# Optimization experiments

Hardware: AMD Instinct MI355X
Metric: run time of the kernel (lower is better)

Reference implementation:

```python
import jax, jax.numpy as jnp
import numpy as np

M, N, K = 1024, 11008, 4096


def _unpack_i2u(Bp):
    """Unpack 2-bit unsigned weights per decode_i2u_to_i8s interleave.

    Bp: [N, K//4] int8 storage. Within each group of 4 bytes (16 elements),
    output element at position 4*i + j = (byte_j >> (2*i)) & 3.
    Returns [N, K] int8 with values in {0,1,2,3}.
    """
    Bu = jax.lax.bitcast_convert_type(Bp, jnp.uint8)  # [N, K//4]
    n, kc = Bu.shape
    Bg = Bu.reshape(n, kc // 4, 1, 4)                 # [N, G, 1, j]
    shifts = (jnp.arange(4, dtype=jnp.uint8) * jnp.uint8(2)).reshape(1, 1, 4, 1)
    vals = (Bg >> shifts) & jnp.uint8(3)              # [N, G, i, j]
    return vals.reshape(n, kc * 4).astype(jnp.int8)   # [N, K]


def setup_inputs() -> dict:
    key = jax.random.key(0)
    k1, k2 = jax.random.split(key)
    A = jax.random.randint(k1, (M, K), -128, 128, dtype=jnp.int8)
    B = jax.random.randint(k2, (N, K // 4), -128, 128, dtype=jnp.int8)
    return {"A": A, "B": B}


def reference(A, B):
    W = _unpack_i2u(B)  # [N, K] int8
    C = jax.lax.dot_general(
        A, W,
        dimension_numbers=(((1,), (1,)), ((), ())),
        preferred_element_type=jnp.int32,
    )  # [M, N] int32
    return C
```

## Files before the change

### kernel.cpp

```cpp
#include <hip/hip_runtime.h>
#include <stdint.h>


#define MM 1024
#define NN 11008
#define KK 4096
#define MTILES 8
#define NTILES 86
#define NBLOCKS (MTILES * NTILES)
#define STRIDE_A ((size_t)MTILES * 8192)
#define STRIDE_B ((size_t)NTILES * 2048)

using i32x4  = __attribute__((ext_vector_type(4))) int;
using i32x16 = __attribute__((ext_vector_type(16))) int;

__device__ __forceinline__ int pack4(i32x4 v) {
    return (int)(((uint32_t)v[0] & 0xFFu) | (((uint32_t)v[1] & 0xFFu) << 8)
               | (((uint32_t)v[2] & 0xFFu) << 16) | (((uint32_t)v[3] & 0xFFu) << 24));
}

__global__ __launch_bounds__(256) void prep_AB(const int* __restrict__ Asrc,
                                               const int* __restrict__ Bsrc,
                                               uint8_t* __restrict__ A2,
                                               uint8_t* __restrict__ B3) {
    if (blockIdx.x < 1024) {
        const int g = blockIdx.x * 256 + threadIdx.x;
        const int kstep = g >> 12;
        const int rem   = g & 4095;
        const int mtile = rem >> 9;
        const int c     = rem & 511;
        const int row32 = (c >> 7) & 3, kk2 = (c >> 6) & 1;
        const int lane  = c & 63;
        const int row   = mtile * 128 + row32 * 32 + (lane & 31);
        const int kbyte = kstep * 64 + kk2 * 32 + (lane >> 5) * 16;
        const i32x4* s4 = (const i32x4*)(Asrc + (size_t)row * KK + kbyte);
        i32x4 o;
#pragma unroll
        for (int q = 0; q < 4; ++q) o[q] = pack4(s4[q]);
        *(i32x4*)(A2 + (size_t)g * 16) = o;
    } else {
        const int t = (blockIdx.x - 1024) * 256 + threadIdx.x;
        const int n = t >> 6, kstep = t & 63;
        const int ntile = n >> 7, hf = (n >> 6) & 1, ni = (n >> 5) & 1, l31 = n & 31;
        const i32x4* s4 = (const i32x4*)(Bsrc + (size_t)n * (KK / 4) + kstep * 16);
        int w[4];
#pragma unroll
        for (int j = 0; j < 4; ++j) w[j] = pack4(s4[j]);
        uint8_t* base = B3 + ((size_t)kstep * NTILES + ntile) * 2048 + hf * 1024;
        *(int2*)(base + l31 * 16 + ni * 8)        = make_int2(w[0], w[2]);
        *(int2*)(base + (l31 + 32) * 16 + ni * 8) = make_int2(w[1], w[3]);
    }
}

#define GLOAD_LDS16(g, l) __builtin_amdgcn_global_load_lds(                    \
        (const __attribute__((address_space(1))) uint32_t*)(g),                \
        (__attribute__((address_space(3))) uint32_t*)(l), 16, 0, 0)

#define MFMA_I8 __builtin_amdgcn_mfma_i32_32x32x32_i8

#define PSTAGE(T) do {                                                         \
    const uint8_t* at_ = gA + (size_t)(T) * STRIDE_A;                          \
    const uint8_t* bt_ = gB + (size_t)(T) * STRIDE_B;                          \
    uint8_t* l_ = &As[(T) % 5][0];                                             \
    GLOAD_LDS16(at_,        l_);                                               \
    GLOAD_LDS16(at_ + 1024, l_ + 1024);                                        \
    GLOAD_LDS16(at_ + 2048, l_ + 2048);                                        \
    GLOAD_LDS16(at_ + 3072, l_ + 3072);                                        \
    GLOAD_LDS16(at_ + 4096, l_ + 4096);                                        \
    GLOAD_LDS16(at_ + 5120, l_ + 5120);                                        \
    GLOAD_LDS16(at_ + 6144, l_ + 6144);                                        \
    GLOAD_LDS16(at_ + 7168, l_ + 7168);                                        \
    GLOAD_LDS16(bt_,        l_ + 8192);                                        \
    GLOAD_LDS16(bt_ + 1024, l_ + 9216);                                        \
} while (0)

#define PWAIT(N) asm volatile("s_waitcnt vmcnt(" #N ")" ::: "memory")

#define READF(BUF, T) do {                                                     \
    const uint8_t* ab_ = &As[(T) % 5][0];                                      \
    BUF##_a00 = *(const i32x4*)(ab_ + (wr * 2 + 0) * 2048 + lane * 16);        \
    BUF##_a01 = *(const i32x4*)(ab_ + (wr * 2 + 0) * 2048 + 1024 + lane * 16); \
    BUF##_a10 = *(const i32x4*)(ab_ + (wr * 2 + 1) * 2048 + lane * 16);        \
    BUF##_a11 = *(const i32x4*)(ab_ + (wr * 2 + 1) * 2048 + 1024 + lane * 16); \
    BUF##_bv  = *(const i32x4*)(ab_ + 8192 + wc * 1024 + lane * 16);           \
} while (0)

#define COMPR(BUF) do {                                                        \
    _Pragma("unroll")                                                          \
    for (int kk2_ = 0; kk2_ < 2; ++kk2_) {                                     \
        const uint32_t q0_ = (uint32_t)BUF##_bv[kk2_];                         \
        const uint32_t q1_ = (uint32_t)BUF##_bv[2 + kk2_];                     \
        i32x4 b0_, b1_;                                                        \
        _Pragma("unroll")                                                      \
        for (int i_ = 0; i_ < 4; ++i_) {                                       \
            b0_[i_] = (int)((q0_ >> (2 * i_)) & 0x03030303u);                  \
            b1_[i_] = (int)((q1_ >> (2 * i_)) & 0x03030303u);                  \
        }                                                                      \
        const i32x4 am0_ = kk2_ ? BUF##_a01 : BUF##_a00;                       \
        const i32x4 am1_ = kk2_ ? BUF##_a11 : BUF##_a10;                       \
        acc[0][0] = MFMA_I8(am0_, b0_, acc[0][0], 0, 0, 0);                    \
        acc[0][1] = MFMA_I8(am0_, b1_, acc[0][1], 0, 0, 0);                    \
        acc[1][0] = MFMA_I8(am1_, b0_, acc[1][0], 0, 0, 0);                    \
        acc[1][1] = MFMA_I8(am1_, b1_, acc[1][1], 0, 0, 0);                    \
    }                                                                          \
} while (0)

__global__ __launch_bounds__(320, 3) void bitnet_gemm(const uint8_t* __restrict__ A2,
                                                      const uint8_t* __restrict__ B3,
                                                      int* __restrict__ C) {
    const int tid  = threadIdx.x;
    const int lane = tid & 63, wave = tid >> 6;
    const int wr   = (wave >> 1) & 1, wc = wave & 1;
    const int l31  = lane & 31, h = lane >> 5;

    const int bid = blockIdx.x;
    const int l   = (bid & 7) * (NBLOCKS / 8) + (bid >> 3);
    const int bm  = l & 7;
    const int bn  = l >> 3;

    __shared__ __align__(16) uint8_t As[5][10240];

    if (wave == 4) {
        const uint8_t* gA = A2 + (size_t)bm * 8192 + lane * 16;
        const uint8_t* gB = B3 + (size_t)bn * 2048 + lane * 16;

        PSTAGE(0); PSTAGE(1); PSTAGE(2); PSTAGE(3);
        PWAIT(20);
        __builtin_amdgcn_s_barrier();
#pragma unroll 1
        for (int t = 0; t < 60; t += 4) {
            PSTAGE(t + 4); PWAIT(20); __builtin_amdgcn_s_barrier();
            PSTAGE(t + 5); PWAIT(20); __builtin_amdgcn_s_barrier();
            PSTAGE(t + 6); PWAIT(20); __builtin_amdgcn_s_barrier();
            PSTAGE(t + 7); PWAIT(20); __builtin_amdgcn_s_barrier();
        }
        PWAIT(10); __builtin_amdgcn_s_barrier();
        PWAIT(0);  __builtin_amdgcn_s_barrier();
        __builtin_amdgcn_s_barrier();
        __builtin_amdgcn_s_barrier();
        return;
    }

    i32x16 acc[2][2] = {};
    i32x4 b0_a00, b0_a01, b0_a10, b0_a11, b0_bv;
    i32x4 b1_a00, b1_a01, b1_a10, b1_a11, b1_bv;

    __builtin_amdgcn_s_barrier();
    READF(b0, 0);

#pragma unroll 1
    for (int t = 0; t < 64; t += 2) {
        __builtin_amdgcn_s_barrier();
        if (t + 1 < 64) READF(b1, t + 1);
        COMPR(b0);
        __builtin_amdgcn_s_barrier();
        if (t + 2 < 64) READF(b0, t + 2);
        COMPR(b1);
    }

    const int brow = bm * 128, bcol = bn * 128;
#pragma unroll
    for (int mi = 0; mi < 2; ++mi)
#pragma unroll
        for (int ni = 0; ni < 2; ++ni) {
            const int colg = bcol + wc * 64 + ni * 32 + l31;
#pragma unroll
            for (int r = 0; r < 16; ++r) {
                const int rowin = (r & 3) + 8 * (r >> 2) + 4 * h;
                const int rowg  = brow + wr * 64 + mi * 32 + rowin;
                C[(size_t)rowg * NN + colg] = acc[mi][ni][r];
            }
        }
}

extern "C" void kernel_launch(void* const* d_in, const int* in_sizes, int n_in,
                              void* d_out, int out_size, void* d_ws, size_t ws_size,
                              hipStream_t stream) {
    const int* A32 = (const int*)d_in[0];
    const int* B32 = (const int*)d_in[1];
    int* C = (int*)d_out;

    uint8_t* A2 = (uint8_t*)d_ws;
    uint8_t* B3 = A2 + (size_t)MM * KK;

    prep_AB<<<dim3(1024 + 2752), dim3(256), 0, stream>>>(A32, B32, A2, B3);
    bitnet_gemm<<<dim3(NBLOCKS), dim3(320), 0, stream>>>(A2, B3, C);
}
```

Baseline: 66.59 us.

## Shrink LDS pipeline to four stages and reorder B prep indexing

The GEMM's producer-wave pipeline drops from five LDS stages to four, prefetching three stages ahead. Buffer indexing becomes a cheap mask instead of a modulo, and the consumer loop's last iteration is peeled to remove in-loop conditionals. Cutting LDS per block from 50 KB to 40 KB may allow more resident blocks per CU, in exchange for less prefetch slack. The B prep kernel also swaps its thread mapping so that n varies fastest, which changes the coalescing of both its reads and its writes.

```diff
diff --git a/kernel.cpp b/kernel.cpp
--- a/kernel.cpp
+++ b/kernel.cpp
@@ -40,7 +40,8 @@
         *(i32x4*)(A2 + (size_t)g * 16) = o;
     } else {
         const int t = (blockIdx.x - 1024) * 256 + threadIdx.x;
-        const int n = t >> 6, kstep = t & 63;
+        const int kstep = t / NN;
+        const int n     = t - kstep * NN;
         const int ntile = n >> 7, hf = (n >> 6) & 1, ni = (n >> 5) & 1, l31 = n & 31;
         const i32x4* s4 = (const i32x4*)(Bsrc + (size_t)n * (KK / 4) + kstep * 16);
         int w[4];
@@ -61,7 +62,7 @@
 #define PSTAGE(T) do {                                                         \
     const uint8_t* at_ = gA + (size_t)(T) * STRIDE_A;                          \
     const uint8_t* bt_ = gB + (size_t)(T) * STRIDE_B;                          \
-    uint8_t* l_ = &As[(T) % 5][0];                                             \
+    uint8_t* l_ = &As[(T) & 3][0];                                             \
     GLOAD_LDS16(at_,        l_);                                               \
     GLOAD_LDS16(at_ + 1024, l_ + 1024);                                        \
     GLOAD_LDS16(at_ + 2048, l_ + 2048);                                        \
@@ -75,9 +76,10 @@
 } while (0)
 
 #define PWAIT(N) asm volatile("s_waitcnt vmcnt(" #N ")" ::: "memory")
+#define BAR()    __builtin_amdgcn_s_barrier()
 
 #define READF(BUF, T) do {                                                     \
-    const uint8_t* ab_ = &As[(T) % 5][0];                                      \
+    const uint8_t* ab_ = &As[(T) & 3][0];                                      \
     BUF##_a00 = *(const i32x4*)(ab_ + (wr * 2 + 0) * 2048 + lane * 16);        \
     BUF##_a01 = *(const i32x4*)(ab_ + (wr * 2 + 0) * 2048 + 1024 + lane * 16); \
     BUF##_a10 = *(const i32x4*)(ab_ + (wr * 2 + 1) * 2048 + lane * 16);        \
@@ -118,26 +120,26 @@
     const int bm  = l & 7;
     const int bn  = l >> 3;
 
-    __shared__ __align__(16) uint8_t As[5][10240];
+    __shared__ __align__(16) uint8_t As[4][10240];
 
     if (wave == 4) {
         const uint8_t* gA = A2 + (size_t)bm * 8192 + lane * 16;
         const uint8_t* gB = B3 + (size_t)bn * 2048 + lane * 16;
 
-        PSTAGE(0); PSTAGE(1); PSTAGE(2); PSTAGE(3);
-        PWAIT(20);
-        __builtin_amdgcn_s_barrier();
+        PSTAGE(0); PSTAGE(1); PSTAGE(2);
+        PWAIT(10);
+        BAR();
 #pragma unroll 1
         for (int t = 0; t < 60; t += 4) {
-            PSTAGE(t + 4); PWAIT(20); __builtin_amdgcn_s_barrier();
-            PSTAGE(t + 5); PWAIT(20); __builtin_amdgcn_s_barrier();
-            PSTAGE(t + 6); PWAIT(20); __builtin_amdgcn_s_barrier();
-            PSTAGE(t + 7); PWAIT(20); __builtin_amdgcn_s_barrier();
+            PSTAGE(t + 3); PWAIT(10); BAR();
+            PSTAGE(t + 4); PWAIT(10); BAR();
+            PSTAGE(t + 5); PWAIT(10); BAR();
+            PSTAGE(t + 6); PWAIT(10); BAR();
         }
-        PWAIT(10); __builtin_amdgcn_s_barrier();
-        PWAIT(0);  __builtin_amdgcn_s_barrier();
-        __builtin_amdgcn_s_barrier();
-        __builtin_amdgcn_s_barrier();
+        PSTAGE(63); PWAIT(10); BAR();
+        PWAIT(0);  BAR();
+        BAR();
+        BAR();
         return;
     }
 
@@ -145,18 +147,23 @@
     i32x4 b0_a00, b0_a01, b0_a10, b0_a11, b0_bv;
     i32x4 b1_a00, b1_a01, b1_a10, b1_a11, b1_bv;
 
-    __builtin_amdgcn_s_barrier();
+    BAR();
     READF(b0, 0);
 
 #pragma unroll 1
-    for (int t = 0; t < 64; t += 2) {
-        __builtin_amdgcn_s_barrier();
-        if (t + 1 < 64) READF(b1, t + 1);
+    for (int t = 0; t < 62; t += 2) {
+        BAR();
+        READF(b1, t + 1);
         COMPR(b0);
-        __builtin_amdgcn_s_barrier();
-        if (t + 2 < 64) READF(b0, t + 2);
+        BAR();
+        READF(b0, t + 2);
         COMPR(b1);
     }
+    BAR();
+    READF(b1, 63);
+    COMPR(b0);
+    BAR();
+    COMPR(b1);
 
     const int brow = bm * 128, bcol = bn * 128;
 #pragma unroll
```

Result: slower. 71.86 us (+7.9%).
